# Optimization experiments

Measured on AMD Instinct MI355X. Metric: run time of the kernel, lower is better.

Reference implementation:

```python
import jax, jax.numpy as jnp
import numpy as np

N = 8192
DIN = 256
DOUT = 128
ALPHA = 0.2      # leaky-relu negative slope
K_MAX = 32       # static upper bound on action.max()+1 (action in [0, 32))
NEG_BIG = -9.0e15


def setup_inputs() -> dict:
    key = jax.random.key(0)
    ks = jax.random.split(key, 6)
    xavier_w = 1.414 * np.sqrt(6.0 / (DIN + DOUT))
    xavier_a = 1.414 * np.sqrt(6.0 / (DOUT + 1))
    return {
        "input": jax.random.normal(ks[0], (N, DIN), dtype=jnp.float32),
        "adj": jax.random.randint(ks[1], (N, N), 0, 2, dtype=jnp.int32),
        "action": jax.random.randint(ks[2], (N,), 0, K_MAX, dtype=jnp.int32),
        "W": jax.random.uniform(ks[3], (DIN, DOUT), jnp.float32, -xavier_w, xavier_w),
        "a_self": jax.random.uniform(ks[4], (DOUT, 1), jnp.float32, -xavier_a, xavier_a),
        "a_neighs": jax.random.uniform(ks[5], (DOUT, 1), jnp.float32, -xavier_a, xavier_a),
        "breadth_policy": 1,
    }


def reference(input, adj, action, W, a_self, a_neighs, breadth_policy):
    h = input @ W                                  # [N, DOUT]
    attn_self = h @ a_self                         # [N, 1]
    attn_neighs = h @ a_neighs                     # [N, 1]
    e = jax.nn.leaky_relu(attn_self + attn_neighs.T, negative_slope=ALPHA)  # [N, N]
    masked = jnp.where(adj > 0, e, jnp.float32(NEG_BIG))
    attention = jax.nn.softmax(masked, axis=1)     # [N, N]
    if breadth_policy:
        # static K_MAX >= action.max()+1; thresholds only read index action[i]
        top_vals, _ = jax.lax.top_k(attention, K_MAX)          # [N, K_MAX], sorted desc
        thresholds = top_vals[jnp.arange(N), action]           # [N]
        attention = jnp.where(attention < thresholds[:, None], 0.0, attention)
    h_prime = attention @ h                        # [N, DOUT]
    return jax.nn.elu(h_prime)                     # concat=True
```

## Files before the change

### kernel.cpp

```cpp
#include <hip/hip_runtime.h>
#include <cstdint>
#include <cstddef>

#define NN   8192
#define DIN  256
#define DOUT 128
#define LRA  0.2f

__global__ __launch_bounds__(256) void gemm_h_kernel(
    const float* __restrict__ input, const float* __restrict__ W,
    float* __restrict__ h)
{
    __shared__ float tile[16][DIN];
    const int row0 = blockIdx.x * 16;
    {
        const float4* in4 = (const float4*)(input + (size_t)row0 * DIN);
        float4* t4 = (float4*)&tile[0][0];
        for (int k = threadIdx.x; k < 16 * DIN / 4; k += 256) t4[k] = in4[k];
    }
    __syncthreads();
    const int c = threadIdx.x & 127;
    const int g = threadIdx.x >> 7;
    float acc[8] = {0.f, 0.f, 0.f, 0.f, 0.f, 0.f, 0.f, 0.f};
    #pragma unroll 2
    for (int k = 0; k < DIN; k += 4) {
        const float w0 = W[(k + 0) * DOUT + c];
        const float w1 = W[(k + 1) * DOUT + c];
        const float w2 = W[(k + 2) * DOUT + c];
        const float w3 = W[(k + 3) * DOUT + c];
        #pragma unroll
        for (int m = 0; m < 8; ++m) {
            const float4 av = *(const float4*)&tile[g * 8 + m][k];
            acc[m] += av.x * w0 + av.y * w1 + av.z * w2 + av.w * w3;
        }
    }
    #pragma unroll
    for (int m = 0; m < 8; ++m)
        h[(size_t)(row0 + g * 8 + m) * DOUT + c] = acc[m];
}

__global__ __launch_bounds__(256) void attn_vec_kernel(
    const float* __restrict__ h, const float* __restrict__ a_self,
    const float* __restrict__ a_neighs, float* __restrict__ s,
    float* __restrict__ t)
{
    const int wid  = (blockIdx.x * 256 + threadIdx.x) >> 6;
    const int lane = threadIdx.x & 63;
    if (wid >= NN) return;
    const float h0 = h[(size_t)wid * DOUT + lane];
    const float h1 = h[(size_t)wid * DOUT + 64 + lane];
    float vs = h0 * a_self[lane]   + h1 * a_self[64 + lane];
    float vn = h0 * a_neighs[lane] + h1 * a_neighs[64 + lane];
    for (int off = 32; off > 0; off >>= 1) {
        vs += __shfl_down(vs, off);
        vn += __shfl_down(vn, off);
    }
    if (lane == 0) { s[wid] = vs; t[wid] = vn; }
}

__global__ __launch_bounds__(256) void rank_kernel(
    const float* __restrict__ t, int* __restrict__ order)
{
    __shared__ float tl[NN];
    __shared__ int   part[8][32];
    for (int k = threadIdx.x; k < NN; k += 256) tl[k] = t[k];
    __syncthreads();
    const int jloc = threadIdx.x & 31;
    const int seg  = threadIdx.x >> 5;
    const int j    = blockIdx.x * 32 + jloc;
    const float tj = tl[j];
    int r = 0;
    const int k0 = seg * (NN / 8);
    const float4* tl4 = (const float4*)(tl + k0);
    #pragma unroll 4
    for (int k = 0; k < NN / 8 / 4; ++k) {
        const float4 tv = tl4[k];
        const int kb = k0 + 4 * k;
        r += (tv.x > tj) ? 1 : ((tv.x == tj && (kb + 0) < j) ? 1 : 0);
        r += (tv.y > tj) ? 1 : ((tv.y == tj && (kb + 1) < j) ? 1 : 0);
        r += (tv.z > tj) ? 1 : ((tv.z == tj && (kb + 2) < j) ? 1 : 0);
        r += (tv.w > tj) ? 1 : ((tv.w == tj && (kb + 3) < j) ? 1 : 0);
    }
    part[seg][jloc] = r;
    __syncthreads();
    if (threadIdx.x < 32) {
        int rr = 0;
        #pragma unroll
        for (int ss = 0; ss < 8; ++ss) rr += part[ss][threadIdx.x];
        order[rr] = blockIdx.x * 32 + threadIdx.x;
    }
}

__global__ __launch_bounds__(256) void gat_row_kernel(
    const int* __restrict__ adj, const float* __restrict__ s_arr,
    const float* __restrict__ t_arr, const int* __restrict__ order,
    const int* __restrict__ action, const float* __restrict__ h,
    const int* __restrict__ policy, float* __restrict__ out)
{
    __shared__ int   ord_s[256];
    __shared__ float ts_s[256];
    __shared__ float red4[4];
    __shared__ float numlds[2][128];
    __shared__ int   sel_j[64];
    __shared__ float sel_w[64];
    __shared__ int   sel_cnt_sh;
    __shared__ int   done_sh;

    const int row = blockIdx.x;
    const int tid = threadIdx.x;

    {
        const int oj = order[tid];
        ord_s[tid] = oj;
        ts_s[tid]  = t_arr[oj];
    }
    __syncthreads();

    const float s    = s_arr[row];
    const float tmax = ts_s[0];
    const float zc   = s + tmax;
    const float C    = fmaxf(zc, LRA * zc);

    const int4*   arow = (const int4*)(adj + (size_t)row * NN);
    const float4* t4   = (const float4*)t_arr;
    float acc = 0.f;
    #pragma unroll
    for (int k = 0; k < 8; ++k) {
        const int idx = tid + k * 256;
        const int4   a  = arow[idx];
        const float4 tv = t4[idx];
        float z, e, w;
        z = s + tv.x; e = fmaxf(z, LRA * z); w = __expf(e - C); if (a.x > 0) acc += w;
        z = s + tv.y; e = fmaxf(z, LRA * z); w = __expf(e - C); if (a.y > 0) acc += w;
        z = s + tv.z; e = fmaxf(z, LRA * z); w = __expf(e - C); if (a.z > 0) acc += w;
        z = s + tv.w; e = fmaxf(z, LRA * z); w = __expf(e - C); if (a.w > 0) acc += w;
    }
    #pragma unroll
    for (int off = 32; off > 0; off >>= 1) acc += __shfl_down(acc, off);
    if ((tid & 63) == 0) red4[tid >> 6] = acc;
    __syncthreads();
    const float l = red4[0] + red4[1] + red4[2] + red4[3];

    int K = action[row] + 1;
    if (policy[0] == 0) K = 0x7FFFFFFF;
    const int c = tid & 127;
    const int g = tid >> 7;
    float accv = 0.f, accv2 = 0.f;

    const int lane = tid & 63;
    float tthr = -3.0e38f;
    int found = 0;
    int cnt = 0;
    int base = 0;

    while (true) {
        if (tid < 64) {
            const int p = base + lane;
            int j = 0, valid = 0;
            float tj = -3.0e38f;
            if (p < NN) {
                if (p < 256) { j = ord_s[p]; tj = ts_s[p]; }
                else         { j = order[p]; tj = t_arr[j]; }
                valid = (adj[(size_t)row * NN + j] > 0) ? 1 : 0;
            }
            const unsigned long long vm = __ballot(valid);
            if (!found) {
                const int cv = __popcll(vm);
                if (cnt + cv >= K) {
                    const int need = K - cnt;
                    const int myrank =
                        __popcll(vm & ((1ull << lane) - 1ull)) + 1;
                    const unsigned long long pm =
                        __ballot(valid && (myrank == need));
                    const int L = __ffsll((long long)pm) - 1;
                    tthr  = __shfl(tj, L);
                    found = 1;
                } else {
                    cnt += cv;
                }
            }
            const int selected = valid && (tj >= tthr);
            const unsigned long long sm = __ballot(selected);
            const int pos = __popcll(sm & ((1ull << lane) - 1ull));
            if (selected) {
                const float z = s + tj;
                const float e = fmaxf(z, LRA * z);
                sel_j[pos] = j;
                sel_w[pos] = __expf(e - C);
            }
            if (lane == 0) {
                sel_cnt_sh = __popcll(sm);
                const int nb = base + 64;
                int dn;
                if (nb >= NN) dn = 1;
                else if (found) {
                    const float tnb = (nb < 256) ? ts_s[nb] : t_arr[order[nb]];
                    dn = (tnb < tthr) ? 1 : 0;
                } else dn = 0;
                done_sh = dn;
            }
        }
        __syncthreads();
        const int nsel = sel_cnt_sh;
        const int dn   = done_sh;
        for (int e2 = g; e2 < nsel; e2 += 4) {
            const float w0 = sel_w[e2];
            const float v0 = h[(size_t)sel_j[e2] * DOUT + c];
            if (e2 + 2 < nsel) {
                accv2 += sel_w[e2 + 2] * h[(size_t)sel_j[e2 + 2] * DOUT + c];
            }
            accv += w0 * v0;
        }
        base += 64;
        if (dn) break;
        __syncthreads();
    }
    accv += accv2;

    numlds[g][c] = accv;
    __syncthreads();
    if (tid < 128) {
        const float v = (numlds[0][tid] + numlds[1][tid]) / l;
        out[(size_t)row * DOUT + tid] = (v > 0.f) ? v : expm1f(v);
    }
}

extern "C" void kernel_launch(void* const* d_in, const int* in_sizes, int n_in,
                              void* d_out, int out_size, void* d_ws,
                              size_t ws_size, hipStream_t stream)
{
    const float* input    = (const float*)d_in[0];
    const int*   adj      = (const int*)d_in[1];
    const int*   action   = (const int*)d_in[2];
    const float* W        = (const float*)d_in[3];
    const float* a_self   = (const float*)d_in[4];
    const float* a_neighs = (const float*)d_in[5];
    const int*   policy   = (const int*)d_in[6];
    float* out = (float*)d_out;

    float* ws    = (float*)d_ws;
    float* h     = ws;
    float* s     = ws + (size_t)NN * DOUT;
    float* t     = s + NN;
    int*   order = (int*)(t + NN);

    hipLaunchKernelGGL(gemm_h_kernel, dim3(512), dim3(256), 0, stream,
                       input, W, h);
    hipLaunchKernelGGL(attn_vec_kernel, dim3(2048), dim3(256), 0, stream,
                       h, a_self, a_neighs, s, t);
    hipLaunchKernelGGL(rank_kernel, dim3(256), dim3(256), 0, stream,
                       t, order);
    hipLaunchKernelGGL(gat_row_kernel, dim3(8192), dim3(256), 0, stream,
                       adj, s, t, order, action, h, policy, out);
}
```

Measured before the change: 426.9 us.

## Fuse attention-vector dots into GEMM, widen gather ILP, defer order staging

Each GEMM thread now computes two adjacent output columns, and the kernel computes the s and t attention dot products in its epilogue using wave shuffles. This removes the separate attn_vec kernel and its re-read of h. In the row kernel, staging the top-256 order entries into shared memory moves after the adjacency pass so that its latency overlaps, and tmax is read directly from global memory. The weighted neighbour gather keeps four independent accumulators with clamped indices instead of two, giving more loads in flight at the cost of a few redundant loads on tail iterations.

```diff
diff --git a/kernel.cpp b/kernel.cpp
--- a/kernel.cpp
+++ b/kernel.cpp
@@ -7,9 +7,10 @@
 #define DOUT 128
 #define LRA  0.2f
 
-__global__ __launch_bounds__(256) void gemm_h_kernel(
+__global__ __launch_bounds__(256) void gemm_h_fused_kernel(
     const float* __restrict__ input, const float* __restrict__ W,
-    float* __restrict__ h)
+    const float* __restrict__ a_self, const float* __restrict__ a_neighs,
+    float* __restrict__ h, float* __restrict__ s, float* __restrict__ t)
 {
     __shared__ float tile[16][DIN];
     const int row0 = blockIdx.x * 16;
@@ -19,43 +20,39 @@
         for (int k = threadIdx.x; k < 16 * DIN / 4; k += 256) t4[k] = in4[k];
     }
     __syncthreads();
-    const int c = threadIdx.x & 127;
-    const int g = threadIdx.x >> 7;
-    float acc[8] = {0.f, 0.f, 0.f, 0.f, 0.f, 0.f, 0.f, 0.f};
+    const int c2 = (threadIdx.x & 63) * 2;
+    const int g  = threadIdx.x >> 6;
+    float2 acc[4];
+    #pragma unroll
+    for (int m = 0; m < 4; ++m) acc[m] = make_float2(0.f, 0.f);
     #pragma unroll 2
     for (int k = 0; k < DIN; k += 4) {
-        const float w0 = W[(k + 0) * DOUT + c];
-        const float w1 = W[(k + 1) * DOUT + c];
-        const float w2 = W[(k + 2) * DOUT + c];
-        const float w3 = W[(k + 3) * DOUT + c];
+        const float2 w0 = *(const float2*)&W[(k + 0) * DOUT + c2];
+        const float2 w1 = *(const float2*)&W[(k + 1) * DOUT + c2];
+        const float2 w2 = *(const float2*)&W[(k + 2) * DOUT + c2];
+        const float2 w3 = *(const float2*)&W[(k + 3) * DOUT + c2];
         #pragma unroll
-        for (int m = 0; m < 8; ++m) {
-            const float4 av = *(const float4*)&tile[g * 8 + m][k];
-            acc[m] += av.x * w0 + av.y * w1 + av.z * w2 + av.w * w3;
-        }
-    }
-    #pragma unroll
-    for (int m = 0; m < 8; ++m)
-        h[(size_t)(row0 + g * 8 + m) * DOUT + c] = acc[m];
-}
-
-__global__ __launch_bounds__(256) void attn_vec_kernel(
-    const float* __restrict__ h, const float* __restrict__ a_self,
-    const float* __restrict__ a_neighs, float* __restrict__ s,
-    float* __restrict__ t)
-{
-    const int wid  = (blockIdx.x * 256 + threadIdx.x) >> 6;
-    const int lane = threadIdx.x & 63;
-    if (wid >= NN) return;
-    const float h0 = h[(size_t)wid * DOUT + lane];
-    const float h1 = h[(size_t)wid * DOUT + 64 + lane];
-    float vs = h0 * a_self[lane]   + h1 * a_self[64 + lane];
-    float vn = h0 * a_neighs[lane] + h1 * a_neighs[64 + lane];
-    for (int off = 32; off > 0; off >>= 1) {
-        vs += __shfl_down(vs, off);
-        vn += __shfl_down(vn, off);
-    }
-    if (lane == 0) { s[wid] = vs; t[wid] = vn; }
+        for (int m = 0; m < 4; ++m) {
+            const float4 av = *(const float4*)&tile[g * 4 + m][k];
+            acc[m].x += av.x * w0.x + av.y * w1.x + av.z * w2.x + av.w * w3.x;
+            acc[m].y += av.x * w0.y + av.y * w1.y + av.z * w2.y + av.w * w3.y;
+        }
+    }
+    const float as0 = a_self[c2],   as1 = a_self[c2 + 1];
+    const float an0 = a_neighs[c2], an1 = a_neighs[c2 + 1];
+    #pragma unroll
+    for (int m = 0; m < 4; ++m) {
+        const int row = row0 + g * 4 + m;
+        *(float2*)&h[(size_t)row * DOUT + c2] = acc[m];
+        float vs = acc[m].x * as0 + acc[m].y * as1;
+        float vn = acc[m].x * an0 + acc[m].y * an1;
+        #pragma unroll
+        for (int off = 32; off > 0; off >>= 1) {
+            vs += __shfl_down(vs, off);
+            vn += __shfl_down(vn, off);
+        }
+        if ((threadIdx.x & 63) == 0) { s[row] = vs; t[row] = vn; }
+    }
 }
 
 __global__ __launch_bounds__(256) void rank_kernel(
@@ -109,15 +106,8 @@
     const int row = blockIdx.x;
     const int tid = threadIdx.x;
 
-    {
-        const int oj = order[tid];
-        ord_s[tid] = oj;
-        ts_s[tid]  = t_arr[oj];
-    }
-    __syncthreads();
-
     const float s    = s_arr[row];
-    const float tmax = ts_s[0];
+    const float tmax = t_arr[order[0]];
     const float zc   = s + tmax;
     const float C    = fmaxf(zc, LRA * zc);
 
@@ -135,6 +125,11 @@
         z = s + tv.z; e = fmaxf(z, LRA * z); w = __expf(e - C); if (a.z > 0) acc += w;
         z = s + tv.w; e = fmaxf(z, LRA * z); w = __expf(e - C); if (a.w > 0) acc += w;
     }
+    {
+        const int oj = order[tid];
+        ord_s[tid] = oj;
+        ts_s[tid]  = t_arr[oj];
+    }
     #pragma unroll
     for (int off = 32; off > 0; off >>= 1) acc += __shfl_down(acc, off);
     if ((tid & 63) == 0) red4[tid >> 6] = acc;
@@ -145,7 +140,7 @@
     if (policy[0] == 0) K = 0x7FFFFFFF;
     const int c = tid & 127;
     const int g = tid >> 7;
-    float accv = 0.f, accv2 = 0.f;
+    float a0 = 0.f, a1 = 0.f, a2 = 0.f, a3 = 0.f;
 
     const int lane = tid & 63;
     float tthr = -3.0e38f;
@@ -203,19 +198,26 @@
         __syncthreads();
         const int nsel = sel_cnt_sh;
         const int dn   = done_sh;
-        for (int e2 = g; e2 < nsel; e2 += 4) {
-            const float w0 = sel_w[e2];
-            const float v0 = h[(size_t)sel_j[e2] * DOUT + c];
-            if (e2 + 2 < nsel) {
-                accv2 += sel_w[e2 + 2] * h[(size_t)sel_j[e2 + 2] * DOUT + c];
-            }
-            accv += w0 * v0;
+        for (int e2 = g; e2 < nsel; e2 += 8) {
+            const int e2b = e2 + 2, e2c = e2 + 4, e2d = e2 + 6;
+            const int jA = sel_j[e2];
+            const int jB = sel_j[(e2b < nsel) ? e2b : e2];
+            const int jC = sel_j[(e2c < nsel) ? e2c : e2];
+            const int jD = sel_j[(e2d < nsel) ? e2d : e2];
+            const float wA = sel_w[e2];
+            const float wB = (e2b < nsel) ? sel_w[e2b] : 0.f;
+            const float wC = (e2c < nsel) ? sel_w[e2c] : 0.f;
+            const float wD = (e2d < nsel) ? sel_w[e2d] : 0.f;
+            a0 += wA * h[(size_t)jA * DOUT + c];
+            a1 += wB * h[(size_t)jB * DOUT + c];
+            a2 += wC * h[(size_t)jC * DOUT + c];
+            a3 += wD * h[(size_t)jD * DOUT + c];
         }
         base += 64;
         if (dn) break;
         __syncthreads();
     }
-    accv += accv2;
+    const float accv = (a0 + a1) + (a2 + a3);
 
     numlds[g][c] = accv;
     __syncthreads();
@@ -244,10 +246,8 @@
     float* t     = s + NN;
     int*   order = (int*)(t + NN);
 
-    hipLaunchKernelGGL(gemm_h_kernel, dim3(512), dim3(256), 0, stream,
-                       input, W, h);
-    hipLaunchKernelGGL(attn_vec_kernel, dim3(2048), dim3(256), 0, stream,
-                       h, a_self, a_neighs, s, t);
+    hipLaunchKernelGGL(gemm_h_fused_kernel, dim3(512), dim3(256), 0, stream,
+                       input, W, a_self, a_neighs, h, s, t);
     hipLaunchKernelGGL(rank_kernel, dim3(256), dim3(256), 0, stream,
                        t, order);
     hipLaunchKernelGGL(gat_row_kernel, dim3(8192), dim3(256), 0, stream,
```

New measurement: 428.2 us. About the same (+0.3%).
